# Kernel tuning notes

Measured on AMD Instinct MI355X. Metric: run time of the kernel, lower is better.

## Reference

```python
import jax, jax.numpy as jnp
import numpy as np

COEF = 0.3989422917366028


def setup_inputs() -> dict:
    key = jax.random.key(0)
    ks = jax.random.split(key, 5)
    B, T, D, E, H = 64, 2048, 512, 1024, 102  # H = mem_elem // 10
    query = jax.random.normal(ks[0], (B, E), dtype=jnp.float32)
    inputs = jax.random.normal(ks[1], (B, T, D), dtype=jnp.float32)
    mu_tm1 = jnp.zeros((B, 1), dtype=jnp.float32)
    W1 = jax.random.normal(ks[2], (E, H), dtype=jnp.float32) * 0.02
    b1 = jnp.zeros((H,), dtype=jnp.float32)
    W2 = jax.random.normal(ks[3], (H, 2), dtype=jnp.float32) * 0.02
    b2 = jnp.zeros((2,), dtype=jnp.float32)
    return {"query": query, "inputs": inputs, "mu_tm1": mu_tm1,
            "W1": W1, "b1": b1, "W2": W2, "b2": b2}


def reference(query, inputs, mu_tm1, W1, b1, W2, b2):
    # N_a: Linear -> ReLU -> Linear, output [B, 2]
    gbk = jax.nn.relu(query @ W1 + b1) @ W2 + b2
    b_t = gbk[:, 0]                     # [B]
    k_t = gbk[:, 1:2]                   # [B, 1]
    sig_t = jax.nn.sigmoid(b_t) * 0.5 + 0.5        # [B]
    mu_t = mu_tm1 + jax.nn.sigmoid(k_t)             # [B, 1]
    T = inputs.shape[1]
    J = jnp.arange(T, dtype=jnp.float32)            # [T]
    # Gaussian scores over memory positions
    phi = jnp.exp(-0.5 * sig_t[:, None] * (mu_t - J[None, :]) ** 2)  # [B, T]
    alpha = COEF * phi + 1e-8
    alpha = alpha / jnp.sum(alpha, axis=1, keepdims=True)  # normalize_attention=True
    c_t = jnp.einsum('bt,btd->bd', alpha, inputs)   # [B, D]
    return c_t
```

## Files before the change

kernel.cpp:

```cpp
#include <hip/hip_runtime.h>
#include <cmath>

#define BB 64
#define TT 2048
#define DD 512
#define EE 1024
#define HH 102
#define MAXW 29
#define COEF 0.3989422917366028f

__device__ __forceinline__ float sigmoidf_(float x) { return 1.0f / (1.0f + expf(-x)); }

__global__ __launch_bounds__(1024) void k_fused(const float* __restrict__ query,
                                                const float* __restrict__ x,
                                                const float* __restrict__ mu_tm1,
                                                const float* __restrict__ W1,
                                                const float* __restrict__ b1,
                                                const float* __restrict__ W2,
                                                const float* __restrict__ b2,
                                                float* __restrict__ out) {
    __shared__ float4 xw4[MAXW * (DD / 4)];
    __shared__ float  qs[EE];
    __shared__ float  hidp[16][HH];
    __shared__ float  hid[HH];
    __shared__ float  al[32];
    float* xw = (float*)xw4;

    const int b   = blockIdx.x;
    const int tid = threadIdx.x;

    if (tid < EE / 4) ((float4*)qs)[tid] = ((const float4*)(query + (size_t)b * EE))[tid];
    __syncthreads();

    {
        const int sl = tid >> 6;
        const int hp = tid & 63;
        if (hp < 51) {
            const float* qp = qs + sl * 64;
            const float* wbase = W1 + (size_t)sl * 64 * HH + 2 * hp;
            float a0 = 0.f, a1 = 0.f, a2 = 0.f, a3 = 0.f;
            #pragma unroll 8
            for (int e = 0; e < 64; e += 2) {
                const float2 w0 = *(const float2*)(wbase + (size_t)e * HH);
                const float2 w1 = *(const float2*)(wbase + (size_t)(e + 1) * HH);
                a0 = fmaf(qp[e],     w0.x, a0);
                a1 = fmaf(qp[e],     w0.y, a1);
                a2 = fmaf(qp[e + 1], w1.x, a2);
                a3 = fmaf(qp[e + 1], w1.y, a3);
            }
            hidp[sl][2 * hp]     = a0 + a2;
            hidp[sl][2 * hp + 1] = a1 + a3;
        }
    }
    __syncthreads();
    if (tid < HH) {
        float s = b1[tid];
        #pragma unroll
        for (int sl = 0; sl < 16; ++sl) s += hidp[sl][tid];
        hid[tid] = fmaxf(s, 0.f);
    }
    __syncthreads();

    if (tid < 64) {
        float p0 = 0.f, p1 = 0.f;
        for (int h = tid; h < HH; h += 64) {
            const float hv = hid[h];
            p0 = fmaf(hv, W2[2 * h + 0], p0);
            p1 = fmaf(hv, W2[2 * h + 1], p1);
        }
        for (int m = 32; m >= 1; m >>= 1) {
            p0 += __shfl_xor(p0, m, 64);
            p1 += __shfl_xor(p1, m, 64);
        }
        const float sig = sigmoidf_(p0 + b2[0]) * 0.5f + 0.5f;
        const float mu  = mu_tm1[b] + sigmoidf_(p1 + b2[1]);

        const float w = ceilf(sqrtf(90.0f / sig));
        int j0 = max(0, (int)ceilf(mu - w));
        j0 = min(j0, TT - 1);
        const int j1 = min(TT - 1, (int)floorf(mu + w));
        const int n  = max(1, min(j1 - j0 + 1, MAXW));

        float ph = 0.f;
        if (tid < n) {
            const float dd = mu - (float)(j0 + tid);
            ph = expf(-0.5f * sig * dd * dd);
        }
        float sp = ph;
        for (int m = 32; m >= 1; m >>= 1) sp += __shfl_xor(sp, m, 64);
        const float Z = COEF * sp + (float)TT * 1e-8f;

        if (tid == 0) { al[0] = (float)j0; al[1] = (float)n; }
        if (tid < MAXW) al[2 + tid] = (tid < n) ? (COEF * ph + 1e-8f) / Z : 0.f;
    }
    __syncthreads();

    const int j0 = (int)al[0];
    const int n  = (int)al[1];
    {
        const int r = tid >> 7;
        const int c = tid & 127;
        const float4* xb4 = (const float4*)(x + ((size_t)b * TT + (size_t)j0) * DD);
        #pragma unroll
        for (int k8 = 0; k8 < (MAXW + 7) / 8; ++k8) {
            const int k = k8 * 8 + r;
            if (k < n) xw4[k * (DD / 4) + c] = xb4[(size_t)k * (DD / 4) + c];
        }
    }
    __syncthreads();

    if (tid < DD) {
        float acc = 0.f;
        for (int k = 0; k < n; ++k)
            acc = fmaf(al[2 + k], xw[k * DD + tid], acc);
        out[(size_t)b * DD + tid] = acc;
    }
}

extern "C" void kernel_launch(void* const* d_in, const int* in_sizes, int n_in,
                              void* d_out, int out_size, void* d_ws, size_t ws_size,
                              hipStream_t stream) {
    const float* query  = (const float*)d_in[0];
    const float* x      = (const float*)d_in[1];
    const float* mu_tm1 = (const float*)d_in[2];
    const float* W1     = (const float*)d_in[3];
    const float* b1     = (const float*)d_in[4];
    const float* W2     = (const float*)d_in[5];
    const float* b2     = (const float*)d_in[6];
    float* out = (float*)d_out;

    hipLaunchKernelGGL(k_fused, dim3(BB), dim3(1024), 0, stream,
                       query, x, mu_tm1, W1, b1, W2, b2, out);
}
```

Baseline: 15.61 us.

## Prefetch input window from mu_tm1 before the MLP to overlap loads

```diff
diff --git a/kernel.cpp b/kernel.cpp
--- a/kernel.cpp
+++ b/kernel.cpp
@@ -6,7 +6,7 @@
 #define DD 512
 #define EE 1024
 #define HH 102
-#define MAXW 29
+#define PF 32
 #define COEF 0.3989422917366028f
 
 __device__ __forceinline__ float sigmoidf_(float x) { return 1.0f / (1.0f + expf(-x)); }
@@ -19,17 +19,29 @@
                                                 const float* __restrict__ W2,
                                                 const float* __restrict__ b2,
                                                 float* __restrict__ out) {
-    __shared__ float4 xw4[MAXW * (DD / 4)];
+    __shared__ float4 xw4[PF * (DD / 4)];
     __shared__ float  qs[EE];
     __shared__ float  hidp[16][HH];
     __shared__ float  hid[HH];
     __shared__ float  al[32];
-    float* xw = (float*)xw4;
+    const float* xw = (const float*)xw4;
 
     const int b   = blockIdx.x;
     const int tid = threadIdx.x;
 
+    const float mut = mu_tm1[b];
     if (tid < EE / 4) ((float4*)qs)[tid] = ((const float4*)(query + (size_t)b * EE))[tid];
+
+    const int pbase = min(max((int)floorf(mut) - 14, 0), TT - PF);
+
+    float4 pf0, pf1, pf2, pf3;
+    {
+        const float4* xb4 = (const float4*)(x + ((size_t)b * TT + (size_t)pbase) * DD);
+        pf0 = xb4[tid];
+        pf1 = xb4[tid + 1024];
+        pf2 = xb4[tid + 2048];
+        pf3 = xb4[tid + 3072];
+    }
     __syncthreads();
 
     {
@@ -52,7 +64,13 @@
             hidp[sl][2 * hp + 1] = a1 + a3;
         }
     }
+
+    xw4[tid]        = pf0;
+    xw4[tid + 1024] = pf1;
+    xw4[tid + 2048] = pf2;
+    xw4[tid + 3072] = pf3;
     __syncthreads();
+
     if (tid < HH) {
         float s = b1[tid];
         #pragma unroll
@@ -73,13 +91,13 @@
             p1 += __shfl_xor(p1, m, 64);
         }
         const float sig = sigmoidf_(p0 + b2[0]) * 0.5f + 0.5f;
-        const float mu  = mu_tm1[b] + sigmoidf_(p1 + b2[1]);
+        const float mu  = mut + sigmoidf_(p1 + b2[1]);
 
         const float w = ceilf(sqrtf(90.0f / sig));
         int j0 = max(0, (int)ceilf(mu - w));
         j0 = min(j0, TT - 1);
         const int j1 = min(TT - 1, (int)floorf(mu + w));
-        const int n  = max(1, min(j1 - j0 + 1, MAXW));
+        const int n  = max(1, min(j1 - j0 + 1, 29));
 
         float ph = 0.f;
         if (tid < n) {
@@ -90,29 +108,17 @@
         for (int m = 32; m >= 1; m >>= 1) sp += __shfl_xor(sp, m, 64);
         const float Z = COEF * sp + (float)TT * 1e-8f;
 
-        if (tid == 0) { al[0] = (float)j0; al[1] = (float)n; }
-        if (tid < MAXW) al[2 + tid] = (tid < n) ? (COEF * ph + 1e-8f) / Z : 0.f;
+        if (tid == 0) { al[0] = (float)(j0 - pbase); al[1] = (float)n; }
+        if (tid < 29) al[2 + tid] = (tid < n) ? (COEF * ph + 1e-8f) / Z : 0.f;
     }
     __syncthreads();
 
-    const int j0 = (int)al[0];
+    const int r0 = (int)al[0];
     const int n  = (int)al[1];
-    {
-        const int r = tid >> 7;
-        const int c = tid & 127;
-        const float4* xb4 = (const float4*)(x + ((size_t)b * TT + (size_t)j0) * DD);
-        #pragma unroll
-        for (int k8 = 0; k8 < (MAXW + 7) / 8; ++k8) {
-            const int k = k8 * 8 + r;
-            if (k < n) xw4[k * (DD / 4) + c] = xb4[(size_t)k * (DD / 4) + c];
-        }
-    }
-    __syncthreads();
-
     if (tid < DD) {
         float acc = 0.f;
         for (int k = 0; k < n; ++k)
-            acc = fmaf(al[2 + k], xw[k * DD + tid], acc);
+            acc = fmaf(al[2 + k], xw[(r0 + k) * DD + tid], acc);
         out[(size_t)b * DD + tid] = acc;
     }
 }
```

Measured after the change: 15.64 us. Within noise of the previous version (+0.2%).
